# Optimization experiments

Measured on AMD Instinct MI355X. Metric: run time of the kernel, lower is better.

The kernel has to match this reference:

```python
import jax, jax.numpy as jnp
import numpy as np

NUM_ITERATIONS = 3
EPS = 1e-7

def squash(v, axis=-1):
    # scale = |v|^2/(1+|v|^2) * v/sqrt(|v|^2+eps), matching the torch module
    sq = jnp.sum(v * v, axis=axis, keepdims=True)
    return (sq / (1.0 + sq)) * v / jnp.sqrt(sq + EPS)

def setup_inputs() -> dict:
    key = jax.random.key(0)
    kx, kw = jax.random.split(key)
    B, R, C, O, I = 256, 1152, 10, 16, 8
    x = jax.random.normal(kx, (B, R, I), dtype=jnp.float32)
    W = jax.random.normal(kw, (R, C, O, I), dtype=jnp.float32)
    return {"x": x, "W": W}

def reference(x, W):
    B, R, I = x.shape
    C, O = W.shape[1], W.shape[2]
    # u_hat[b,r,c,o] = sum_i W[r,c,o,i] * x[b,r,i]  (batched tiny GEMV)
    u_hat = jnp.einsum('rcoi,bri->brco', W, x)
    b_ij = jnp.zeros((B, R, C), dtype=u_hat.dtype)
    v = None
    for it in range(NUM_ITERATIONS):
        c_ij = jax.nn.softmax(b_ij, axis=1)          # softmax over route nodes (dim=1, as in source)
        s_j = jnp.einsum('brc,brco->bco', c_ij, u_hat)
        v = squash(s_j, axis=-1)                      # squash over out_channels (dim=-2 of the 5D torch tensor)
        if it != NUM_ITERATIONS - 1:
            b_ij = b_ij + jnp.einsum('brco,bco->brc', u_hat, v)
    # match torch output shape (B, 1, C, O, 1)
    return v[:, None, :, :, None]
```

## Files before the change

kernel.cpp:

```cpp
#include <hip/hip_runtime.h>
#include <cstdint>

#define BB 256
#define RR 1152
#define CC 10
#define OO 16
#define II 8
#define NT 768
#define GG 2
#define NWAVE (NT / 64)
#define WPG (NWAVE / GG)
#define LOG2E 1.4426950408889634f

typedef float float2v __attribute__((ext_vector_type(2)));

__device__ __forceinline__ void unpack2(uint32_t pk, float& lo, float& hi) {
    union { uint32_t i; float f; } a, b;
    a.i = pk << 16; b.i = pk & 0xffff0000u;
    lo = a.f; hi = b.f;
}
__device__ __forceinline__ float dot4pk(float4 a, float4 b) {
    float2v al = { a.x, a.y }, ah = { a.z, a.w };
    float2v bl = { b.x, b.y }, bh = { b.z, b.w };
    float2v h = __builtin_elementwise_fma(ah, bh, al * bl);
    return h.x + h.y;
}
__device__ __forceinline__ float qpadd1(float v) {
    int o = __builtin_amdgcn_mov_dpp(__float_as_int(v), 0xB1, 0xF, 0xF, true);
    return v + __int_as_float(o);
}
__device__ __forceinline__ float qpadd2(float v) {
    int o = __builtin_amdgcn_mov_dpp(__float_as_int(v), 0x4E, 0xF, 0xF, true);
    return v + __int_as_float(o);
}
__device__ __forceinline__ float dppx2f(float v) {
    return __int_as_float(__builtin_amdgcn_mov_dpp(__float_as_int(v), 0x4E, 0xF, 0xF, true));
}
__device__ __forceinline__ uint32_t cvtpk(float lo, float hi) {
    uint32_t r;
    asm("v_cvt_pk_bf16_f32 %0, %1, %2" : "=v"(r) : "v"(lo), "v"(hi));
    return r;
}
#if __has_builtin(__builtin_amdgcn_exp2f)
#define EXP2(x) __builtin_amdgcn_exp2f(x)
#else
#define EXP2(x) __expf((x) * 0.6931471805599453f)
#endif
#define LD4(P) (*reinterpret_cast<const float4*>(P))

#define P1G(XV, SG0, SG1, SG2, SG3, WR)                                       \
  do {                                                                        \
    float d0 = qpadd1(dot4pk(w0, XV));                                        \
    float d1 = qpadd1(dot4pk(w1, XV));                                        \
    float d2 = qpadd1(dot4pk(w2, XV));                                        \
    float d3 = qpadd1(dot4pk(w3, XV));                                        \
    SG0 += d0; SG1 += d1; SG2 += d2; SG3 += d3;                               \
    float sa = pb1 ? (pb0 ? d3 : d2) : (pb0 ? d1 : d0);                       \
    float sb = pb1 ? (pb0 ? d1 : d0) : (pb0 ? d3 : d2);                       \
    (WR)[(size_t)it * 768] = cvtpk(sa, dppx2f(sb));                           \
  } while (0)

__global__ __launch_bounds__(NT, 6)
void k_caps(const float* __restrict__ x, const float* __restrict__ W,
            float* __restrict__ out) {
    extern __shared__ uint32_t u2[];
    __shared__ float p0s[NWAVE][8][4][GG];
    __shared__ float part2[2][17][NWAVE];

    const int t = threadIdx.x;
    const int c  = blockIdx.x / (BB / GG);
    const int b0 = (blockIdx.x % (BB / GG)) * GG;
    const int wv = t >> 6, l = t & 63;
    const int rg = t >> 3, p = t & 7;

    uint32_t* uA = u2;
    uint32_t* uB = u2 + (size_t)RR * 8;

    const int pos = (p >> 1) + ((p & 1) << 2);
    uint32_t* wrA = uA + (size_t)rg * 8 + pos;
    uint32_t* wrB = uB + (size_t)rg * 8 + pos;
    const bool pb0 = (p & 1) != 0, pb1 = (p & 2) != 0;

    float s00 = 0.f, s01 = 0.f, s02 = 0.f, s03 = 0.f;
    float s10 = 0.f, s11 = 0.f, s12 = 0.f, s13 = 0.f;
#pragma unroll 2
    for (int it = 0; it < 12; ++it) {
        const int r = it * 96 + rg;
        const float* wrow = W + ((size_t)r * CC + c) * (OO * II) + p * 4;
        float4 w0 = LD4(wrow);
        float4 w1 = LD4(wrow + 32);
        float4 w2 = LD4(wrow + 64);
        float4 w3 = LD4(wrow + 96);
        const float* xp = x + ((size_t)b0 * RR + r) * II + (p & 1) * 4;
        float4 xa = LD4(xp);
        float4 xb = LD4(xp + (size_t)RR * II);
        P1G(xa, s00, s01, s02, s03, wrA);
        P1G(xb, s10, s11, s12, s13, wrB);
    }
#pragma unroll
    for (int m = 8; m < 64; m <<= 1) {
        s00 += __shfl_xor(s00, m); s01 += __shfl_xor(s01, m);
        s02 += __shfl_xor(s02, m); s03 += __shfl_xor(s03, m);
        s10 += __shfl_xor(s10, m); s11 += __shfl_xor(s11, m);
        s12 += __shfl_xor(s12, m); s13 += __shfl_xor(s13, m);
    }
    if (l < 8) {
        p0s[wv][l][0][0] = s00; p0s[wv][l][1][0] = s01;
        p0s[wv][l][2][0] = s02; p0s[wv][l][3][0] = s03;
        p0s[wv][l][0][1] = s10; p0s[wv][l][1][1] = s11;
        p0s[wv][l][2][1] = s12; p0s[wv][l][3][1] = s13;
    }
    __syncthreads();

    const int g2 = wv / WPG;
    const int wv6 = wv - g2 * WPG;
    const uint32_t* ug = g2 ? uB : uA;
    const int q = l & 3;
    const int rl = l >> 2;
    const int rbase = wv6 * 16 + rl;
    const uint32_t* rp = ug + (size_t)rbase * 8 + 2 * q;

    const int oo = l & 15;
    const int gb = l & 48;
    const int t0 = gb | (2 * q), t1 = gb | (2 * q + 1);
    const int t2 = gb | (2 * q + 8), t3 = gb | (2 * q + 9);

    float ra, rb, rc, rd;
    {
        float sv = 0.f;
#pragma unroll
        for (int w = 0; w < NWAVE; ++w) sv += p0s[w][2 * (oo & 3)][oo >> 2][g2];
        sv *= (1.0f / RR);
        float ss = sv * sv;
        ss += __shfl_xor(ss, 1); ss += __shfl_xor(ss, 2);
        ss += __shfl_xor(ss, 4); ss += __shfl_xor(ss, 8);
        float vv = sv * (ss / ((1.0f + ss) * sqrtf(ss + 1e-7f)));
        ra = __shfl(vv, t0); rb = __shfl(vv, t1);
        rc = __shfl(vv, t2); rd = __shfl(vv, t3);
    }

#pragma unroll
    for (int pass = 1; pass < 3; ++pass) {
        const float2v WQA = { ra * LOG2E, rc * LOG2E };
        const float2v WQB = { rb * LOG2E, rd * LOG2E };
        float2v N0 = { 0.f, 0.f }, N1 = { 0.f, 0.f };
        float den = 0.f;

#pragma unroll
        for (int it2 = 0; it2 < 12; ++it2) {
            uint2 pp = *reinterpret_cast<const uint2*>(rp + (size_t)it2 * 768);
            float u0, u1, u2f, u3;
            unpack2(pp.x, u0, u1);
            unpack2(pp.y, u3, u2f);
            float2v P0 = { u0, u2f };
            float2v P1 = { u1, u3 };
            float2v lg2 = __builtin_elementwise_fma(P0, WQA, P1 * WQB);
            float lg = lg2.x + lg2.y;
            lg = qpadd1(lg);
            lg = qpadd2(lg);
            float e = EXP2(lg);
            den += e;
            float2v E2 = { e, e };
            N0 = __builtin_elementwise_fma(E2, P0, N0);
            N1 = __builtin_elementwise_fma(E2, P1, N1);
        }

        float n0 = N0.x, n2 = N0.y, n1 = N1.x, n3 = N1.y;
#pragma unroll
        for (int m = 4; m < 64; m <<= 1) {
            n0 += __shfl_xor(n0, m); n1 += __shfl_xor(n1, m);
            n2 += __shfl_xor(n2, m); n3 += __shfl_xor(n3, m);
            den += __shfl_xor(den, m);
        }
        const int pb = pass & 1;
        if (l < 4) {
            part2[pb][2 * l][wv]     = n0;
            part2[pb][2 * l + 1][wv] = n1;
            part2[pb][2 * l + 8][wv] = n2;
            part2[pb][2 * l + 9][wv] = n3;
            if (l == 0) part2[pb][16][wv] = den;
        }
        __syncthreads();

        const float* po = &part2[pb][oo][0];
        const float* pd = &part2[pb][16][0];
        float nf = 0.f, df = 0.f;
#pragma unroll
        for (int w = 0; w < WPG; ++w) {
            nf += po[g2 * WPG + w];
            df += pd[g2 * WPG + w];
        }
        float s2 = nf / df;
        float ss2 = s2 * s2;
        ss2 += __shfl_xor(ss2, 1); ss2 += __shfl_xor(ss2, 2);
        ss2 += __shfl_xor(ss2, 4); ss2 += __shfl_xor(ss2, 8);
        float vv2 = s2 * (ss2 / ((1.0f + ss2) * sqrtf(ss2 + 1e-7f)));

        if (pass == 1) {
            ra += __shfl(vv2, t0); rb += __shfl(vv2, t1);
            rc += __shfl(vv2, t2); rd += __shfl(vv2, t3);
        } else {
            if ((wv == 0 || wv == WPG) && l < 16)
                out[((size_t)(b0 + g2) * CC + c) * OO + oo] = vv2;
        }
    }
}

extern "C" void kernel_launch(void* const* d_in, const int* in_sizes, int n_in,
                              void* d_out, int out_size, void* d_ws, size_t ws_size,
                              hipStream_t stream) {
    const float* x = (const float*)d_in[0];
    const float* W = (const float*)d_in[1];
    if (n_in >= 2 && in_sizes[0] == RR * CC * OO * II &&
        in_sizes[1] == BB * RR * II) {
        const float* tmp = x; x = W; W = tmp;
    }
    float* out = (float*)d_out;

    const size_t dyn_lds = (size_t)GG * RR * 8 * 4;
    k_caps<<<CC * (BB / GG), NT, dyn_lds, stream>>>(x, W, out);
}
```

Baseline: 109.7 us.

## Pre-convert W to bf16 in a separate kernel and restructure GEMV lane mapping

Adds a pre-pass kernel that converts W from fp32 to packed bf16 in the workspace, so the main kernel reads half as many bytes of W across its 1280 blocks. The GEMV is remapped so each lane computes full 8-element dot products for two output channels, with no cross-lane DPP reduction, and the LDS u_hat layout and index math change to match. This costs an extra launch plus a full read and write of W on every call, and uses bf16 weights in the u_hat computation, which lowers precision.

```diff
diff --git a/kernel.cpp b/kernel.cpp
--- a/kernel.cpp
+++ b/kernel.cpp
@@ -11,6 +11,7 @@
 #define NWAVE (NT / 64)
 #define WPG (NWAVE / GG)
 #define LOG2E 1.4426950408889634f
+#define WSWORDS ((size_t)RR * CC * (OO * II / 2))
 
 typedef float float2v __attribute__((ext_vector_type(2)));
 
@@ -19,12 +20,6 @@
     a.i = pk << 16; b.i = pk & 0xffff0000u;
     lo = a.f; hi = b.f;
 }
-__device__ __forceinline__ float dot4pk(float4 a, float4 b) {
-    float2v al = { a.x, a.y }, ah = { a.z, a.w };
-    float2v bl = { b.x, b.y }, bh = { b.z, b.w };
-    float2v h = __builtin_elementwise_fma(ah, bh, al * bl);
-    return h.x + h.y;
-}
 __device__ __forceinline__ float qpadd1(float v) {
     int o = __builtin_amdgcn_mov_dpp(__float_as_int(v), 0xB1, 0xF, 0xF, true);
     return v + __int_as_float(o);
@@ -32,9 +27,6 @@
 __device__ __forceinline__ float qpadd2(float v) {
     int o = __builtin_amdgcn_mov_dpp(__float_as_int(v), 0x4E, 0xF, 0xF, true);
     return v + __int_as_float(o);
-}
-__device__ __forceinline__ float dppx2f(float v) {
-    return __int_as_float(__builtin_amdgcn_mov_dpp(__float_as_int(v), 0x4E, 0xF, 0xF, true));
 }
 __device__ __forceinline__ uint32_t cvtpk(float lo, float hi) {
     uint32_t r;
@@ -48,23 +40,42 @@
 #endif
 #define LD4(P) (*reinterpret_cast<const float4*>(P))
 
-#define P1G(XV, SG0, SG1, SG2, SG3, WR)                                       \
+#define DOT8(PA0, PA1, PA2, PA3, X0, X1, X2, X3, OUT)                         \
   do {                                                                        \
-    float d0 = qpadd1(dot4pk(w0, XV));                                        \
-    float d1 = qpadd1(dot4pk(w1, XV));                                        \
-    float d2 = qpadd1(dot4pk(w2, XV));                                        \
-    float d3 = qpadd1(dot4pk(w3, XV));                                        \
-    SG0 += d0; SG1 += d1; SG2 += d2; SG3 += d3;                               \
-    float sa = pb1 ? (pb0 ? d3 : d2) : (pb0 ? d1 : d0);                       \
-    float sb = pb1 ? (pb0 ? d1 : d0) : (pb0 ? d3 : d2);                       \
-    (WR)[(size_t)it * 768] = cvtpk(sa, dppx2f(sb));                           \
+    float2v acc_ = PA0 * X0;                                                  \
+    acc_ = __builtin_elementwise_fma(PA1, X1, acc_);                          \
+    acc_ = __builtin_elementwise_fma(PA2, X2, acc_);                          \
+    acc_ = __builtin_elementwise_fma(PA3, X3, acc_);                          \
+    OUT = acc_.x + acc_.y;                                                    \
   } while (0)
 
+#define UNPK(WQ, P0, P1, P2, P3)                                              \
+  do {                                                                        \
+    float lo_, hi_;                                                           \
+    unpack2(WQ.x, lo_, hi_); P0 = (float2v){lo_, hi_};                        \
+    unpack2(WQ.y, lo_, hi_); P1 = (float2v){lo_, hi_};                        \
+    unpack2(WQ.z, lo_, hi_); P2 = (float2v){lo_, hi_};                        \
+    unpack2(WQ.w, lo_, hi_); P3 = (float2v){lo_, hi_};                        \
+  } while (0)
+
+__global__ __launch_bounds__(256)
+void k_cvt(const float* __restrict__ Wf, uint32_t* __restrict__ wbf) {
+    size_t i = ((size_t)blockIdx.x * 256 + threadIdx.x) * 4;
+    if (i < WSWORDS) {
+        float4 a = LD4(Wf + 2 * i);
+        float4 b = LD4(Wf + 2 * i + 4);
+        uint4 r;
+        r.x = cvtpk(a.x, a.y); r.y = cvtpk(a.z, a.w);
+        r.z = cvtpk(b.x, b.y); r.w = cvtpk(b.z, b.w);
+        *reinterpret_cast<uint4*>(wbf + i) = r;
+    }
+}
+
 __global__ __launch_bounds__(NT, 6)
-void k_caps(const float* __restrict__ x, const float* __restrict__ W,
+void k_caps(const float* __restrict__ x, const uint32_t* __restrict__ wb,
             float* __restrict__ out) {
     extern __shared__ uint32_t u2[];
-    __shared__ float p0s[NWAVE][8][4][GG];
+    __shared__ float p0s[NWAVE][8][2][GG];
     __shared__ float part2[2][17][NWAVE];
 
     const int t = threadIdx.x;
@@ -75,40 +86,45 @@
 
     uint32_t* uA = u2;
     uint32_t* uB = u2 + (size_t)RR * 8;
-
-    const int pos = (p >> 1) + ((p & 1) << 2);
-    uint32_t* wrA = uA + (size_t)rg * 8 + pos;
-    uint32_t* wrB = uB + (size_t)rg * 8 + pos;
-    const bool pb0 = (p & 1) != 0, pb1 = (p & 2) != 0;
-
-    float s00 = 0.f, s01 = 0.f, s02 = 0.f, s03 = 0.f;
-    float s10 = 0.f, s11 = 0.f, s12 = 0.f, s13 = 0.f;
+    uint32_t* wrA = uA + (size_t)rg * 8 + p;
+    uint32_t* wrB = uB + (size_t)rg * 8 + p;
+
+    float s00 = 0.f, s01 = 0.f, s10 = 0.f, s11 = 0.f;
 #pragma unroll 2
     for (int it = 0; it < 12; ++it) {
         const int r = it * 96 + rg;
-        const float* wrow = W + ((size_t)r * CC + c) * (OO * II) + p * 4;
-        float4 w0 = LD4(wrow);
-        float4 w1 = LD4(wrow + 32);
-        float4 w2 = LD4(wrow + 64);
-        float4 w3 = LD4(wrow + 96);
-        const float* xp = x + ((size_t)b0 * RR + r) * II + (p & 1) * 4;
-        float4 xa = LD4(xp);
-        float4 xb = LD4(xp + (size_t)RR * II);
-        P1G(xa, s00, s01, s02, s03, wrA);
-        P1G(xb, s10, s11, s12, s13, wrB);
+        const uint32_t* wrow = wb + ((size_t)r * CC + c) * 64 + 4 * p;
+        uint4 wq0 = *reinterpret_cast<const uint4*>(wrow);
+        uint4 wq1 = *reinterpret_cast<const uint4*>(wrow + 32);
+        const float* xp = x + ((size_t)b0 * RR + r) * II;
+        float4 xa0 = LD4(xp);
+        float4 xa1 = LD4(xp + 4);
+        float4 xg0 = LD4(xp + (size_t)RR * II);
+        float4 xg1 = LD4(xp + (size_t)RR * II + 4);
+        float2v A0, A1, A2, A3, B0, B1, B2, B3;
+        UNPK(wq0, A0, A1, A2, A3);
+        UNPK(wq1, B0, B1, B2, B3);
+        float2v X0 = { xa0.x, xa0.y }, X1 = { xa0.z, xa0.w };
+        float2v X2 = { xa1.x, xa1.y }, X3 = { xa1.z, xa1.w };
+        float2v Y0 = { xg0.x, xg0.y }, Y1 = { xg0.z, xg0.w };
+        float2v Y2 = { xg1.x, xg1.y }, Y3 = { xg1.z, xg1.w };
+        float d0, d1, e0, e1;
+        DOT8(A0, A1, A2, A3, X0, X1, X2, X3, d0);
+        DOT8(B0, B1, B2, B3, X0, X1, X2, X3, d1);
+        DOT8(A0, A1, A2, A3, Y0, Y1, Y2, Y3, e0);
+        DOT8(B0, B1, B2, B3, Y0, Y1, Y2, Y3, e1);
+        s00 += d0; s01 += d1; s10 += e0; s11 += e1;
+        wrA[(size_t)it * 768] = cvtpk(d0, d1);
+        wrB[(size_t)it * 768] = cvtpk(e0, e1);
     }
 #pragma unroll
     for (int m = 8; m < 64; m <<= 1) {
         s00 += __shfl_xor(s00, m); s01 += __shfl_xor(s01, m);
-        s02 += __shfl_xor(s02, m); s03 += __shfl_xor(s03, m);
         s10 += __shfl_xor(s10, m); s11 += __shfl_xor(s11, m);
-        s12 += __shfl_xor(s12, m); s13 += __shfl_xor(s13, m);
     }
     if (l < 8) {
         p0s[wv][l][0][0] = s00; p0s[wv][l][1][0] = s01;
-        p0s[wv][l][2][0] = s02; p0s[wv][l][3][0] = s03;
         p0s[wv][l][0][1] = s10; p0s[wv][l][1][1] = s11;
-        p0s[wv][l][2][1] = s12; p0s[wv][l][3][1] = s13;
     }
     __syncthreads();
 
@@ -129,7 +145,7 @@
     {
         float sv = 0.f;
 #pragma unroll
-        for (int w = 0; w < NWAVE; ++w) sv += p0s[w][2 * (oo & 3)][oo >> 2][g2];
+        for (int w = 0; w < NWAVE; ++w) sv += p0s[w][oo & 7][oo >> 3][g2];
         sv *= (1.0f / RR);
         float ss = sv * sv;
         ss += __shfl_xor(ss, 1); ss += __shfl_xor(ss, 2);
@@ -149,11 +165,11 @@
 #pragma unroll
         for (int it2 = 0; it2 < 12; ++it2) {
             uint2 pp = *reinterpret_cast<const uint2*>(rp + (size_t)it2 * 768);
-            float u0, u1, u2f, u3;
-            unpack2(pp.x, u0, u1);
-            unpack2(pp.y, u3, u2f);
-            float2v P0 = { u0, u2f };
-            float2v P1 = { u1, u3 };
+            float a_, b_, c_, d_;
+            unpack2(pp.x, a_, b_);
+            unpack2(pp.y, c_, d_);
+            float2v P0 = { a_, b_ };
+            float2v P1 = { c_, d_ };
             float2v lg2 = __builtin_elementwise_fma(P0, WQA, P1 * WQB);
             float lg = lg2.x + lg2.y;
             lg = qpadd1(lg);
@@ -216,7 +232,11 @@
         const float* tmp = x; x = W; W = tmp;
     }
     float* out = (float*)d_out;
+    uint32_t* wbf = (uint32_t*)d_ws;
+
+    const int cvt_blocks = (int)((WSWORDS / 4 + 255) / 256);
+    k_cvt<<<cvt_blocks, 256, 0, stream>>>(W, wbf);
 
     const size_t dyn_lds = (size_t)GG * RR * 8 * 4;
-    k_caps<<<CC * (BB / GG), NT, dyn_lds, stream>>>(x, W, out);
-}
+    k_caps<<<CC * (BB / GG), NT, dyn_lds, stream>>>(x, wbf, out);
+}
```

Result: no change. 110.2 us (+0.4%).
